# Optimization experiments

Measured on AMD Instinct MI355X. Metric: run time of the kernel, lower is better.

The kernel has to match this reference:

```python
import jax, jax.numpy as jnp
import numpy as np

B, HRES, WRES, C, HEADS, WS, SS = 32, 64, 64, 256, 8, 8, 4
N = WS * WS
HID = 4 * C
EPS = 1e-5


def _rel_pos_index(ws):
    coords = np.stack(np.meshgrid(np.arange(ws), np.arange(ws), indexing='ij'))  # [2,ws,ws]
    cf = coords.reshape(2, -1)
    rel = (cf[:, :, None] - cf[:, None, :]).transpose(1, 2, 0)  # [N,N,2]
    rel[:, :, 0] += ws - 1
    rel[:, :, 1] += ws - 1
    rel[:, :, 0] *= 2 * ws - 1
    return rel.sum(-1).reshape(-1)  # [N*N]


def _attn_mask(H, W, ws, ss):
    img = np.zeros((H, W))
    cnt = 0
    for hs in (slice(0, -ws), slice(-ws, -ss), slice(-ss, None)):
        for wsl in (slice(0, -ws), slice(-ws, -ss), slice(-ss, None)):
            img[hs, wsl] = cnt
            cnt += 1
    mw = img.reshape(H // ws, ws, W // ws, ws).transpose(0, 2, 1, 3).reshape(-1, ws * ws)
    am = mw[:, None, :] - mw[:, :, None]  # [nW,N,N]
    return np.where(am != 0, -100.0, 0.0).astype(np.float32)


_RPI = jnp.asarray(_rel_pos_index(WS))
_MASK = jnp.asarray(_attn_mask(HRES, WRES, WS, SS))  # [nW,N,N]


def _ln(x, g, b):
    m = x.mean(-1, keepdims=True)
    v = ((x - m) ** 2).mean(-1, keepdims=True)
    return (x - m) / jnp.sqrt(v + EPS) * g + b


def setup_inputs() -> dict:
    key = jax.random.key(0)
    ks = jax.random.split(key, 16)
    s = 0.02
    return {
        'x': jax.random.normal(ks[0], (B, HRES * WRES, C), jnp.float32),
        'norm1_g': jnp.ones((C,), jnp.float32),
        'norm1_b': jnp.zeros((C,), jnp.float32),
        'qkv_w': jax.random.normal(ks[1], (3 * C, C), jnp.float32) * s,
        'qkv_b': jnp.zeros((3 * C,), jnp.float32),
        'rpb_table': jax.random.normal(ks[2], ((2 * WS - 1) ** 2, HEADS), jnp.float32) * s,
        'proj_w': jax.random.normal(ks[3], (C, C), jnp.float32) * s,
        'proj_b': jnp.zeros((C,), jnp.float32),
        'norm2_g': jnp.ones((C,), jnp.float32),
        'norm2_b': jnp.zeros((C,), jnp.float32),
        'fc1_w': jax.random.normal(ks[4], (HID, C), jnp.float32) * s,
        'fc1_b': jnp.zeros((HID,), jnp.float32),
        'fc2_w': jax.random.normal(ks[5], (C, HID), jnp.float32) * s,
        'fc2_b': jnp.zeros((C,), jnp.float32),
        'H': HRES,
        'W': WRES,
    }


def reference(x, norm1_g, norm1_b, qkv_w, qkv_b, rpb_table, proj_w, proj_b,
              norm2_g, norm2_b, fc1_w, fc1_b, fc2_w, fc2_b, H, W):
    Bn, L, Cd = x.shape
    ws, ss, nh = WS, SS, HEADS
    hd = Cd // nh
    shortcut = x
    h = _ln(x, norm1_g, norm1_b).reshape(Bn, H, W, Cd)
    # cyclic shift (H,W divisible by ws -> no padding needed)
    h = jnp.roll(h, (-ss, -ss), axis=(1, 2))
    # window partition: [B,H,W,C] -> [B*nW, N, C]
    h = h.reshape(Bn, H // ws, ws, W // ws, ws, Cd).transpose(0, 1, 3, 2, 4, 5).reshape(-1, N, Cd)
    qkv = (h @ qkv_w.T + qkv_b).reshape(-1, N, 3, nh, hd).transpose(2, 0, 3, 1, 4)
    q, k, v = qkv[0], qkv[1], qkv[2]  # [B_,h,N,d]
    attn = jnp.einsum('bhnd,bhmd->bhnm', q * (hd ** -0.5), k)
    rpb = rpb_table[_RPI].reshape(N, N, nh).transpose(2, 0, 1)  # [h,N,N]
    attn = attn + rpb[None]
    nW = _MASK.shape[0]
    attn = attn.reshape(Bn, nW, nh, N, N) + _MASK[None, :, None]
    attn = jax.nn.softmax(attn.reshape(-1, nh, N, N), axis=-1)
    o = jnp.einsum('bhnm,bhmd->bhnd', attn, v).transpose(0, 2, 1, 3).reshape(-1, N, Cd)
    o = o @ proj_w.T + proj_b
    # window reverse + reverse shift
    o = o.reshape(Bn, H // ws, W // ws, ws, ws, Cd).transpose(0, 1, 3, 2, 4, 5).reshape(Bn, H, W, Cd)
    o = jnp.roll(o, (ss, ss), axis=(1, 2)).reshape(Bn, L, Cd)
    x = shortcut + o
    h2 = _ln(x, norm2_g, norm2_b)
    h2 = jax.nn.gelu(h2 @ fc1_w.T + fc1_b, approximate=False)
    return x + (h2 @ fc2_w.T + fc2_b)
```

## Files before the change

### kernel.cpp

```cpp
#include <hip/hip_runtime.h>
#include <hip/hip_bf16.h>
#include <stdint.h>

typedef __bf16 bf16_t;
typedef __bf16 bf16x8 __attribute__((ext_vector_type(8)));
typedef __bf16 bf16x4 __attribute__((ext_vector_type(4)));
typedef float f32x4 __attribute__((ext_vector_type(4)));

#define MROWS 131072

__device__ __forceinline__ bf16_t to_bf16(float f) {
  __hip_bfloat16 h = __float2bfloat16(f);
  return *reinterpret_cast<bf16_t*>(&h);
}

__device__ __forceinline__ f32x4 mfma16(bf16x8 a, bf16x8 b, f32x4 c) {
  return __builtin_amdgcn_mfma_f32_16x16x32_bf16(a, b, c, 0, 0, 0);
}

__device__ __forceinline__ void gload16(const void* g, void* l) {
  __builtin_amdgcn_global_load_lds(
      (const __attribute__((address_space(1))) void*)g,
      (__attribute__((address_space(3))) void*)l, 16, 0, 0);
}

__device__ __forceinline__ int map_row(int m) {
  int b   = m >> 12;
  int rem = m & 4095;
  int win = rem >> 6;
  int n   = rem & 63;
  int gh  = ((win >> 3) << 3) + (n >> 3);
  int gw  = ((win & 7) << 3) + (n & 7);
  int sh  = (gh + 4) & 63;
  int sw  = (gw + 4) & 63;
  return (b << 12) + (sh << 6) + sw;
}

__device__ __forceinline__ int regid(int g) { return (g < 56) ? 0 : (g < 60 ? 1 : 2); }

__global__ __launch_bounds__(256) void cvt_kernel(const float* __restrict__ in,
                                                  bf16_t* __restrict__ out, int n) {
  int i = blockIdx.x * 256 + threadIdx.x;
  if (i < n) out[i] = to_bf16(in[i]);
}

template <bool PERM>
__global__ __launch_bounds__(256) void ln_kernel(const float* __restrict__ xin,
                                                 const float* __restrict__ g,
                                                 const float* __restrict__ b,
                                                 bf16_t* __restrict__ out) {
  int row  = (blockIdx.x << 2) + (threadIdx.x >> 6);
  int lane = threadIdx.x & 63;
  int src  = PERM ? map_row(row) : row;
  float4 v = *reinterpret_cast<const float4*>(xin + (size_t)src * 256 + (lane << 2));
  float s = v.x + v.y + v.z + v.w;
#pragma unroll
  for (int d = 1; d < 64; d <<= 1) s += __shfl_xor(s, d);
  float mean = s * 0.00390625f;
  float ax = v.x - mean, ay = v.y - mean, az = v.z - mean, aw = v.w - mean;
  float s2 = ax * ax + ay * ay + az * az + aw * aw;
#pragma unroll
  for (int d = 1; d < 64; d <<= 1) s2 += __shfl_xor(s2, d);
  float rstd = rsqrtf(s2 * 0.00390625f + 1e-5f);
  float4 gv = *reinterpret_cast<const float4*>(g + (lane << 2));
  float4 bv = *reinterpret_cast<const float4*>(b + (lane << 2));
  bf16x4 o4;
  o4[0] = to_bf16(ax * rstd * gv.x + bv.x);
  o4[1] = to_bf16(ay * rstd * gv.y + bv.y);
  o4[2] = to_bf16(az * rstd * gv.z + bv.z);
  o4[3] = to_bf16(aw * rstd * gv.w + bv.w);
  *reinterpret_cast<bf16x4*>(out + (size_t)row * 256 + (lane << 2)) = o4;
}

template <int EPI>
__global__ __launch_bounds__(256) void gemm_bt(const bf16_t* __restrict__ A,
                                               const bf16_t* __restrict__ W,
                                               const float* __restrict__ bias,
                                               void* __restrict__ outp,
                                               const float* __restrict__ resid,
                                               int M, int N, int K) {
  __shared__ __align__(16) bf16_t As[128 * 32];
  __shared__ __align__(16) bf16_t Bs[128 * 32];
  const int tid  = threadIdx.x;
  const int lane = tid & 63, lo = lane & 15, hi = lane >> 4;
  const int wave = tid >> 6;
  const int bm = blockIdx.x << 7, bn = blockIdx.y << 7;
  const int wr = (wave >> 1) << 6, wc = (wave & 1) << 6;
  f32x4 acc[4][4] = {};

  for (int k0 = 0; k0 < K; k0 += 32) {
    __syncthreads();
#pragma unroll
    for (int it = 0; it < 2; ++it) {
      int ch = (it << 8) + tid;
      int r = ch >> 2, kf = (ch & 3) << 3;
      gload16(A + (size_t)(bm + r) * K + (k0 + kf), &As[ch << 3]);
      gload16(W + (size_t)(bn + r) * K + (k0 + kf), &Bs[ch << 3]);
    }
    __syncthreads();
    bf16x8 af[4], bfr[4];
#pragma unroll
    for (int i = 0; i < 4; ++i)
      af[i] = *reinterpret_cast<const bf16x8*>(&As[(wr + (i << 4) + lo) * 32 + (hi << 3)]);
#pragma unroll
    for (int j = 0; j < 4; ++j)
      bfr[j] = *reinterpret_cast<const bf16x8*>(&Bs[(wc + (j << 4) + lo) * 32 + (hi << 3)]);
#pragma unroll
    for (int i = 0; i < 4; ++i)
#pragma unroll
      for (int j = 0; j < 4; ++j)
        acc[i][j] = mfma16(af[i], bfr[j], acc[i][j]);
  }

  float bv[4];
#pragma unroll
  for (int j = 0; j < 4; ++j) bv[j] = bias[bn + wc + (j << 4) + lo];

#pragma unroll
  for (int i = 0; i < 4; ++i) {
#pragma unroll
    for (int r = 0; r < 4; ++r) {
      int row = bm + wr + (i << 4) + (hi << 2) + r;
      if constexpr (EPI == 2) {
        int xr = map_row(row);
        float* o = (float*)outp;
#pragma unroll
        for (int j = 0; j < 4; ++j) {
          int col = bn + wc + (j << 4) + lo;
          size_t idx = (size_t)xr * 256 + col;
          o[idx] = resid[idx] + acc[i][j][r] + bv[j];
        }
      } else if constexpr (EPI == 3) {
        float* o = (float*)outp;
#pragma unroll
        for (int j = 0; j < 4; ++j) {
          int col = bn + wc + (j << 4) + lo;
          size_t idx = (size_t)row * 256 + col;
          o[idx] = o[idx] + acc[i][j][r] + bv[j];
        }
      } else {
        bf16_t* o = (bf16_t*)outp;
#pragma unroll
        for (int j = 0; j < 4; ++j) {
          int col = bn + wc + (j << 4) + lo;
          float v = acc[i][j][r] + bv[j];
          if constexpr (EPI == 1) v = 0.5f * v * (1.0f + erff(v * 0.70710678118654752f));
          o[(size_t)row * N + col] = to_bf16(v);
        }
      }
    }
  }
}

__global__ __launch_bounds__(256) void attn_kernel(const bf16_t* __restrict__ q,
                                                   const bf16_t* __restrict__ k,
                                                   const bf16_t* __restrict__ v,
                                                   const float* __restrict__ rpbt,
                                                   bf16_t* __restrict__ o) {
  __shared__ __align__(16) bf16_t Pl[4][64 * 72];
  __shared__ __align__(16) bf16_t Vt[4][32 * 72];
  const int wave = threadIdx.x >> 6, lane = threadIdx.x & 63;
  const int lo = lane & 15, hi = lane >> 4;
  const int id = (blockIdx.x << 2) + wave;
  const int win = id >> 3, h = id & 7;
  const bf16_t* qb = q + (size_t)win * (64 * 256) + h * 32;
  const bf16_t* kb = k + (size_t)win * (64 * 256) + h * 32;
  const bf16_t* vb = v + (size_t)win * (64 * 256) + h * 32;

  bf16x8 qa[4], ka[4];
#pragma unroll
  for (int i = 0; i < 4; ++i)
    qa[i] = *reinterpret_cast<const bf16x8*>(qb + (size_t)((i << 4) + lo) * 256 + (hi << 3));
#pragma unroll
  for (int j = 0; j < 4; ++j)
    ka[j] = *reinterpret_cast<const bf16x8*>(kb + (size_t)((j << 4) + lo) * 256 + (hi << 3));
  f32x4 s[4][4] = {};
#pragma unroll
  for (int i = 0; i < 4; ++i)
#pragma unroll
    for (int j = 0; j < 4; ++j) s[i][j] = mfma16(qa[i], ka[j], s[i][j]);

#pragma unroll
  for (int it = 0; it < 4; ++it) {
    int ch = (it << 6) + lane;
    int m = ch >> 2, d0 = (ch & 3) << 3;
    bf16x8 v8 = *reinterpret_cast<const bf16x8*>(vb + (size_t)m * 256 + d0);
#pragma unroll
    for (int e = 0; e < 8; ++e) Vt[wave][(d0 + e) * 72 + m] = v8[e];
  }

  const int wh = (win & 63) >> 3, ww = win & 7;
  const float scale = 0.17677669529663687f;
  float pinv[4][4];
#pragma unroll
  for (int i = 0; i < 4; ++i) {
#pragma unroll
    for (int r = 0; r < 4; ++r) {
      int n = (i << 4) + (hi << 2) + r;
      int yn = n >> 3, xn = n & 7;
      int cn = regid(wh * 8 + yn) * 3 + regid(ww * 8 + xn);
      float vals[4], mx = -1e30f;
#pragma unroll
      for (int j = 0; j < 4; ++j) {
        int m = (j << 4) + lo;
        int ym = m >> 3, xm = m & 7;
        int cm = regid(wh * 8 + ym) * 3 + regid(ww * 8 + xm);
        float val = s[i][j][r] * scale + rpbt[((yn - ym + 7) * 15 + (xn - xm + 7)) * 8 + h];
        if (cn != cm) val -= 100.0f;
        vals[j] = val;
        mx = fmaxf(mx, val);
      }
#pragma unroll
      for (int d = 1; d < 16; d <<= 1) mx = fmaxf(mx, __shfl_xor(mx, d));
      float sum = 0.0f;
#pragma unroll
      for (int j = 0; j < 4; ++j) {
        float p = __expf(vals[j] - mx);
        sum += p;
        Pl[wave][n * 72 + (j << 4) + lo] = to_bf16(p);
      }
#pragma unroll
      for (int d = 1; d < 16; d <<= 1) sum += __shfl_xor(sum, d);
      pinv[i][r] = 1.0f / sum;
    }
  }

  f32x4 oa[4][2] = {};
#pragma unroll
  for (int kt = 0; kt < 2; ++kt) {
    bf16x8 pa[4], va[2];
#pragma unroll
    for (int i = 0; i < 4; ++i)
      pa[i] = *reinterpret_cast<const bf16x8*>(&Pl[wave][((i << 4) + lo) * 72 + (kt << 5) + (hi << 3)]);
#pragma unroll
    for (int dt = 0; dt < 2; ++dt)
      va[dt] = *reinterpret_cast<const bf16x8*>(&Vt[wave][((dt << 4) + lo) * 72 + (kt << 5) + (hi << 3)]);
#pragma unroll
    for (int i = 0; i < 4; ++i)
#pragma unroll
      for (int dt = 0; dt < 2; ++dt) oa[i][dt] = mfma16(pa[i], va[dt], oa[i][dt]);
  }

  bf16_t* ob = o + (size_t)win * (64 * 256) + h * 32;
#pragma unroll
  for (int i = 0; i < 4; ++i)
#pragma unroll
    for (int r = 0; r < 4; ++r) {
      int n = (i << 4) + (hi << 2) + r;
      float piv = pinv[i][r];
#pragma unroll
      for (int dt = 0; dt < 2; ++dt)
        ob[(size_t)n * 256 + (dt << 4) + lo] = to_bf16(oa[i][dt][r] * piv);
    }
}

extern "C" void kernel_launch(void* const* d_in, const int* in_sizes, int n_in,
                              void* d_out, int out_size, void* d_ws, size_t ws_size,
                              hipStream_t stream) {
  const float* x      = (const float*)d_in[0];
  const float* n1g    = (const float*)d_in[1];
  const float* n1b    = (const float*)d_in[2];
  const float* qkv_w  = (const float*)d_in[3];
  const float* qkv_b  = (const float*)d_in[4];
  const float* rpbt   = (const float*)d_in[5];
  const float* proj_w = (const float*)d_in[6];
  const float* proj_b = (const float*)d_in[7];
  const float* n2g    = (const float*)d_in[8];
  const float* n2b    = (const float*)d_in[9];
  const float* fc1_w  = (const float*)d_in[10];
  const float* fc1_b  = (const float*)d_in[11];
  const float* fc2_w  = (const float*)d_in[12];
  const float* fc2_b  = (const float*)d_in[13];
  float* out = (float*)d_out;
  char*  ws  = (char*)d_ws;

  const size_t MB64 = 67108864;
  bf16_t* hln  = (bf16_t*)(ws);
  bf16_t* obuf = (bf16_t*)(ws);
  bf16_t* h2   = (bf16_t*)(ws);
  bf16_t* qbuf = (bf16_t*)(ws + MB64);
  bf16_t* x2n  = (bf16_t*)(ws + MB64);
  bf16_t* wb   = (bf16_t*)(ws + 2 * MB64);
  bf16_t* qkv_wb  = wb;
  bf16_t* proj_wb = qkv_wb + 196608;
  bf16_t* fc1_wb  = proj_wb + 65536;
  bf16_t* fc2_wb  = fc1_wb + 262144;
  bf16_t* kbuf = (bf16_t*)d_out;
  bf16_t* vbuf = kbuf + 33554432;

  cvt_kernel<<<768, 256, 0, stream>>>(qkv_w, qkv_wb, 196608);
  cvt_kernel<<<256, 256, 0, stream>>>(proj_w, proj_wb, 65536);
  cvt_kernel<<<1024, 256, 0, stream>>>(fc1_w, fc1_wb, 262144);
  cvt_kernel<<<1024, 256, 0, stream>>>(fc2_w, fc2_wb, 262144);

  ln_kernel<true><<<32768, 256, 0, stream>>>(x, n1g, n1b, hln);

  gemm_bt<0><<<dim3(1024, 2), 256, 0, stream>>>(hln, qkv_wb,              qkv_b,       qbuf, nullptr, MROWS, 256, 256);
  gemm_bt<0><<<dim3(1024, 2), 256, 0, stream>>>(hln, qkv_wb + 256 * 256,  qkv_b + 256, kbuf, nullptr, MROWS, 256, 256);
  gemm_bt<0><<<dim3(1024, 2), 256, 0, stream>>>(hln, qkv_wb + 512 * 256,  qkv_b + 512, vbuf, nullptr, MROWS, 256, 256);

  attn_kernel<<<4096, 256, 0, stream>>>(qbuf, kbuf, vbuf, rpbt, obuf);

  gemm_bt<2><<<dim3(1024, 2), 256, 0, stream>>>(obuf, proj_wb, proj_b, out, x, MROWS, 256, 256);

  ln_kernel<false><<<32768, 256, 0, stream>>>(out, n2g, n2b, x2n);

  for (int c = 0; c < 4; ++c) {
    const bf16_t* xa = x2n + (size_t)c * 32768 * 256;
    gemm_bt<1><<<dim3(256, 8), 256, 0, stream>>>(xa, fc1_wb, fc1_b, h2, nullptr, 32768, 1024, 256);
    gemm_bt<3><<<dim3(256, 2), 256, 0, stream>>>(h2, fc2_wb, fc2_b, out + (size_t)c * 32768 * 256,
                                                 nullptr, 32768, 256, 1024);
  }
}
```

Baseline: 703.9 us.

## Fuse QKV GEMMs, store head-major Q/K/V, precompute attention bias table

The three separate Q/K/V GEMM launches become one N=768 GEMM. Its epilogue writes Q, K and V in a head-major layout, [head][row][32], so each attention wave reads contiguous 64x32 tiles instead of strided rows. A small kernel precomputes combined relative-position bias plus shift-mask tables for the four window classes, replacing per-element index math and region comparisons in the softmax loop. The cost is scattered 2-byte epilogue stores, an extra bias read from global memory per score, and a block-wide sync added in attention.

```diff
diff --git a/kernel.cpp b/kernel.cpp
--- a/kernel.cpp
+++ b/kernel.cpp
@@ -36,12 +36,24 @@
   return (b << 12) + (sh << 6) + sw;
 }
 
-__device__ __forceinline__ int regid(int g) { return (g < 56) ? 0 : (g < 60 ? 1 : 2); }
-
 __global__ __launch_bounds__(256) void cvt_kernel(const float* __restrict__ in,
                                                   bf16_t* __restrict__ out, int n) {
   int i = blockIdx.x * 256 + threadIdx.x;
   if (i < n) out[i] = to_bf16(in[i]);
+}
+
+__global__ __launch_bounds__(256) void bias_kernel(const float* __restrict__ rpbt,
+                                                   float* __restrict__ bias) {
+  int idx = blockIdx.x * 256 + threadIdx.x;
+  int m = idx & 63, n = (idx >> 6) & 63, h = (idx >> 12) & 7, c = idx >> 15;
+  int yn = n >> 3, xn = n & 7, ym = m >> 3, xm = m & 7;
+  float v = rpbt[((yn - ym + 7) * 15 + (xn - xm + 7)) * 8 + h];
+  int rn = (c & 2) ? (yn < 4 ? 1 : 2) : 0;
+  int cn = (c & 1) ? (xn < 4 ? 1 : 2) : 0;
+  int rm = (c & 2) ? (ym < 4 ? 1 : 2) : 0;
+  int cm = (c & 1) ? (xm < 4 ? 1 : 2) : 0;
+  if (rn * 3 + cn != rm * 3 + cm) v -= 100.0f;
+  bias[idx] = v;
 }
 
 template <bool PERM>
@@ -77,6 +89,8 @@
                                                const bf16_t* __restrict__ W,
                                                const float* __restrict__ bias,
                                                void* __restrict__ outp,
+                                               void* __restrict__ outp2,
+                                               void* __restrict__ outp3,
                                                const float* __restrict__ resid,
                                                int M, int N, int K) {
   __shared__ __align__(16) bf16_t As[128 * 32];
@@ -138,6 +152,15 @@
           size_t idx = (size_t)row * 256 + col;
           o[idx] = o[idx] + acc[i][j][r] + bv[j];
         }
+      } else if constexpr (EPI == 4) {
+#pragma unroll
+        for (int j = 0; j < 4; ++j) {
+          int col = bn + wc + (j << 4) + lo;
+          bf16_t* base = (col < 256) ? (bf16_t*)outp
+                        : (col < 512) ? (bf16_t*)outp2 : (bf16_t*)outp3;
+          int hd = (col >> 5) & 7, d = col & 31;
+          base[((size_t)hd * MROWS + row) * 32 + d] = to_bf16(acc[i][j][r] + bv[j]);
+        }
       } else {
         bf16_t* o = (bf16_t*)outp;
 #pragma unroll
@@ -152,10 +175,10 @@
   }
 }
 
-__global__ __launch_bounds__(256) void attn_kernel(const bf16_t* __restrict__ q,
-                                                   const bf16_t* __restrict__ k,
-                                                   const bf16_t* __restrict__ v,
-                                                   const float* __restrict__ rpbt,
+__global__ __launch_bounds__(256) void attn_kernel(const bf16_t* __restrict__ qh,
+                                                   const bf16_t* __restrict__ kh,
+                                                   const bf16_t* __restrict__ vh,
+                                                   const float* __restrict__ bias,
                                                    bf16_t* __restrict__ o) {
   __shared__ __align__(16) bf16_t Pl[4][64 * 72];
   __shared__ __align__(16) bf16_t Vt[4][32 * 72];
@@ -163,50 +186,48 @@
   const int lo = lane & 15, hi = lane >> 4;
   const int id = (blockIdx.x << 2) + wave;
   const int win = id >> 3, h = id & 7;
-  const bf16_t* qb = q + (size_t)win * (64 * 256) + h * 32;
-  const bf16_t* kb = k + (size_t)win * (64 * 256) + h * 32;
-  const bf16_t* vb = v + (size_t)win * (64 * 256) + h * 32;
+  const size_t hb = ((size_t)h * MROWS + (size_t)win * 64) * 32;
+  const bf16_t* qb = qh + hb;
+  const bf16_t* kb = kh + hb;
+  const bf16_t* vb = vh + hb;
+
+  const bf16_t* vbl = vb + lane * 32;
+#pragma unroll
+  for (int c4 = 0; c4 < 4; ++c4) {
+    bf16x8 v8 = *reinterpret_cast<const bf16x8*>(vbl + (c4 << 3));
+#pragma unroll
+    for (int e = 0; e < 8; ++e) Vt[wave][((c4 << 3) + e) * 72 + lane] = v8[e];
+  }
 
   bf16x8 qa[4], ka[4];
 #pragma unroll
   for (int i = 0; i < 4; ++i)
-    qa[i] = *reinterpret_cast<const bf16x8*>(qb + (size_t)((i << 4) + lo) * 256 + (hi << 3));
+    qa[i] = *reinterpret_cast<const bf16x8*>(qb + ((i << 4) + lo) * 32 + (hi << 3));
 #pragma unroll
   for (int j = 0; j < 4; ++j)
-    ka[j] = *reinterpret_cast<const bf16x8*>(kb + (size_t)((j << 4) + lo) * 256 + (hi << 3));
+    ka[j] = *reinterpret_cast<const bf16x8*>(kb + ((j << 4) + lo) * 32 + (hi << 3));
   f32x4 s[4][4] = {};
 #pragma unroll
   for (int i = 0; i < 4; ++i)
 #pragma unroll
     for (int j = 0; j < 4; ++j) s[i][j] = mfma16(qa[i], ka[j], s[i][j]);
 
-#pragma unroll
-  for (int it = 0; it < 4; ++it) {
-    int ch = (it << 6) + lane;
-    int m = ch >> 2, d0 = (ch & 3) << 3;
-    bf16x8 v8 = *reinterpret_cast<const bf16x8*>(vb + (size_t)m * 256 + d0);
-#pragma unroll
-    for (int e = 0; e < 8; ++e) Vt[wave][(d0 + e) * 72 + m] = v8[e];
-  }
-
   const int wh = (win & 63) >> 3, ww = win & 7;
+  const int cls = ((wh == 7) ? 2 : 0) + ((ww == 7) ? 1 : 0);
+  const float* bb = bias + ((size_t)cls * 8 + h) * 4096;
   const float scale = 0.17677669529663687f;
+
   float pinv[4][4];
 #pragma unroll
   for (int i = 0; i < 4; ++i) {
 #pragma unroll
     for (int r = 0; r < 4; ++r) {
       int n = (i << 4) + (hi << 2) + r;
-      int yn = n >> 3, xn = n & 7;
-      int cn = regid(wh * 8 + yn) * 3 + regid(ww * 8 + xn);
+      const float* brow = bb + n * 64 + lo;
       float vals[4], mx = -1e30f;
 #pragma unroll
       for (int j = 0; j < 4; ++j) {
-        int m = (j << 4) + lo;
-        int ym = m >> 3, xm = m & 7;
-        int cm = regid(wh * 8 + ym) * 3 + regid(ww * 8 + xm);
-        float val = s[i][j][r] * scale + rpbt[((yn - ym + 7) * 15 + (xn - xm + 7)) * 8 + h];
-        if (cn != cm) val -= 100.0f;
+        float val = s[i][j][r] * scale + brow[j << 4];
         vals[j] = val;
         mx = fmaxf(mx, val);
       }
@@ -224,6 +245,8 @@
       pinv[i][r] = 1.0f / sum;
     }
   }
+
+  __syncthreads();
 
   f32x4 oa[4][2] = {};
 #pragma unroll
@@ -285,6 +308,7 @@
   bf16_t* proj_wb = qkv_wb + 196608;
   bf16_t* fc1_wb  = proj_wb + 65536;
   bf16_t* fc2_wb  = fc1_wb + 262144;
+  float*  biast   = (float*)(fc2_wb + 262144);
   bf16_t* kbuf = (bf16_t*)d_out;
   bf16_t* vbuf = kbuf + 33554432;
 
@@ -292,23 +316,25 @@
   cvt_kernel<<<256, 256, 0, stream>>>(proj_w, proj_wb, 65536);
   cvt_kernel<<<1024, 256, 0, stream>>>(fc1_w, fc1_wb, 262144);
   cvt_kernel<<<1024, 256, 0, stream>>>(fc2_w, fc2_wb, 262144);
+  bias_kernel<<<512, 256, 0, stream>>>(rpbt, biast);
 
   ln_kernel<true><<<32768, 256, 0, stream>>>(x, n1g, n1b, hln);
 
-  gemm_bt<0><<<dim3(1024, 2), 256, 0, stream>>>(hln, qkv_wb,              qkv_b,       qbuf, nullptr, MROWS, 256, 256);
-  gemm_bt<0><<<dim3(1024, 2), 256, 0, stream>>>(hln, qkv_wb + 256 * 256,  qkv_b + 256, kbuf, nullptr, MROWS, 256, 256);
-  gemm_bt<0><<<dim3(1024, 2), 256, 0, stream>>>(hln, qkv_wb + 512 * 256,  qkv_b + 512, vbuf, nullptr, MROWS, 256, 256);
-
-  attn_kernel<<<4096, 256, 0, stream>>>(qbuf, kbuf, vbuf, rpbt, obuf);
-
-  gemm_bt<2><<<dim3(1024, 2), 256, 0, stream>>>(obuf, proj_wb, proj_b, out, x, MROWS, 256, 256);
+  gemm_bt<4><<<dim3(1024, 6), 256, 0, stream>>>(hln, qkv_wb, qkv_b, qbuf, kbuf, vbuf,
+                                                nullptr, MROWS, 768, 256);
+
+  attn_kernel<<<4096, 256, 0, stream>>>(qbuf, kbuf, vbuf, biast, obuf);
+
+  gemm_bt<2><<<dim3(1024, 2), 256, 0, stream>>>(obuf, proj_wb, proj_b, out, nullptr, nullptr,
+                                                x, MROWS, 256, 256);
 
   ln_kernel<false><<<32768, 256, 0, stream>>>(out, n2g, n2b, x2n);
 
   for (int c = 0; c < 4; ++c) {
     const bf16_t* xa = x2n + (size_t)c * 32768 * 256;
-    gemm_bt<1><<<dim3(256, 8), 256, 0, stream>>>(xa, fc1_wb, fc1_b, h2, nullptr, 32768, 1024, 256);
+    gemm_bt<1><<<dim3(256, 8), 256, 0, stream>>>(xa, fc1_wb, fc1_b, h2, nullptr, nullptr,
+                                                 nullptr, 32768, 1024, 256);
     gemm_bt<3><<<dim3(256, 2), 256, 0, stream>>>(h2, fc2_wb, fc2_b, out + (size_t)c * 32768 * 256,
-                                                 nullptr, 32768, 256, 1024);
-  }
-}
+                                                 nullptr, nullptr, nullptr, 32768, 256, 1024);
+  }
+}
```

After: 681.4 us. -3.2%, faster.
